# Optimization experiments

Measured on AMD Instinct MI355X. Metric: run time of the kernel, lower is better.

Reference implementation:

```python
import jax, jax.numpy as jnp
import numpy as np

N_HASHES = 4
CHUNK = 144


def conv2d(x, w, b, pad):
    y = jax.lax.conv_general_dilated(x, w, (1, 1), [(pad, pad), (pad, pad)],
                                     dimension_numbers=('NCHW', 'OIHW', 'NCHW'))
    return y + b[None, :, None, None]


def resblock(x, w1, b1, w2, b2, ws=None, bs=None):
    # conv3x3 -> ReLU -> conv3x3 + skip (1x1 projection when channels change)
    h = conv2d(x, w1, b1, 1)
    h = jax.nn.relu(h)
    h = conv2d(h, w2, b2, 1)
    skip = x if ws is None else conv2d(x, ws, bs, 0)
    return skip + h


def _forward(feature_dec1, feature_dec2, reference_feature,
             mw1, mb1, mw2, mb2, mws, mbs,
             a1w1, a1b1, a1w2, a1b2, a2w1, a2b1, a2w2, a2b2,
             random_index):
    fd1 = jax.lax.stop_gradient(feature_dec1)  # is_detach=True default
    fd2 = jax.lax.stop_gradient(feature_dec2)
    B, C0, H, W = fd1.shape
    L = H * W
    # embeddings: (B, L, C) with C = C0 // reduction, and (B, L, C0) assemblies
    f1 = resblock(fd1, mw1, mb1, mw2, mb2, mws, mbs).reshape(B, -1, L).transpose(0, 2, 1)
    f2 = resblock(fd2, mw1, mb1, mw2, mb2, mws, mbs).reshape(B, -1, L).transpose(0, 2, 1)
    aux1 = resblock(fd1, a1w1, a1b1, a1w2, a1b2).reshape(B, -1, L).transpose(0, 2, 1)
    refe = resblock(reference_feature, a2w1, a2b1, a2w2, a2b2).reshape(B, -1, L).transpose(0, 2, 1)
    C = f1.shape[-1]
    inv_random_index = jnp.argsort(random_index)
    hb = min(2 * L // CHUNK + (2 * L // CHUNK) % 2, 128)
    f1f2 = jnp.concatenate([f1, f2], axis=1)            # (B, 2L, C)
    # LSH hashing (random rotations drawn with a fixed key, matching randn-per-call in torch)
    rot = jax.random.normal(jax.random.key(42), (C, N_HASHES, hb // 2), dtype=f1f2.dtype)
    rv = jnp.einsum('btf,fhi->bhti', f1f2, rot)
    rv = jnp.concatenate([rv, -rv], axis=-1)
    codes = jnp.argmax(rv, axis=-1)                     # (B, nh, 2L)
    codes = codes + (jnp.arange(N_HASHES) * hb)[None, :, None]
    codes = codes[:, :, random_index].reshape(B, -1)    # (B, nh*2L)
    indices = jnp.argsort(codes, axis=-1)
    undo_sort = jnp.argsort(indices, axis=-1)
    mod_indices = (indices % 2) * L                     # faithful to torch `indices % 2 * L` precedence
    zo = jnp.concatenate([jnp.full((B, L), 0.01, f1.dtype),
                          jnp.full((B, L), 0.99, f1.dtype)], axis=1)
    f1f2_p = f1f2[:, random_index, :]
    q = jnp.take_along_axis(f1f2_p, mod_indices[:, :, None], axis=1)
    zo_p = zo[:, random_index]
    z = jnp.take_along_axis(zo_p, mod_indices, axis=1)
    refw = jnp.concatenate([aux1, refe], axis=1)[:, random_index, :]
    r = jnp.take_along_axis(refw, mod_indices[:, :, None], axis=1)
    rem = (2 * L) % CHUNK
    padding = CHUNK - rem if rem != 0 else 0
    qb = q.reshape(B, N_HASHES, 2 * L, C)
    zb = z.reshape(B, N_HASHES, 2 * L)
    rb = r.reshape(B, N_HASHES, 2 * L, -1)
    if padding:
        qb = jnp.concatenate([qb, qb[:, :, -padding:]], axis=2)
        zb = jnp.concatenate([zb, zb[:, :, -padding:]], axis=2)
        rb = jnp.concatenate([rb, rb[:, :, -padding:]], axis=2)
    k = qb.shape[2] // CHUNK
    qb = qb.reshape(B, N_HASHES, k, CHUNK, C)
    zb = zb.reshape(B, N_HASHES, k, CHUNK)
    rb = rb.reshape(B, N_HASHES, k, CHUNK, -1)
    # F.normalize(p=2, dim=-1, eps=5e-5)
    norm = jnp.sqrt(jnp.sum(qb * qb, axis=-1, keepdims=True))
    km = qb / jnp.maximum(norm, 5e-5)
    adj = lambda x: jnp.concatenate([x, jnp.roll(x, 1, axis=2), jnp.roll(x, -1, axis=2)], axis=3)
    km, zb3, rb3 = adj(km), adj(zb), adj(rb)            # keys/vals over 3 adjacent buckets
    raw = jnp.einsum('bhkie,bhkje->bhkij', qb, km)      # (B,nh,k,144,432)
    w = jnp.exp(raw) * zb3[:, :, :, None, :]
    denom = jnp.sum(w, axis=-1, keepdims=True)
    score = w / denom
    bucket_score = denom.reshape(B, N_HASHES, -1)
    ret = jnp.einsum('bhkij,bhkje->bhkie', score, rb3)  # (B,nh,k,144,C0)
    CR = rb3.shape[-1]
    ret = ret.reshape(B, N_HASHES, -1, CR)
    if padding:
        ret = ret[:, :, :-padding]
        bucket_score = bucket_score[:, :, :-padding]
    ret = ret.reshape(B, N_HASHES * 2 * L, CR)
    bucket_score = bucket_score.reshape(B, -1)
    ret = jnp.take_along_axis(ret, undo_sort[:, :, None], axis=1)
    bucket_score = jnp.take_along_axis(bucket_score, undo_sort, axis=1)
    ret = ret.reshape(B, N_HASHES, 2 * L, CR)
    bucket_score = bucket_score.reshape(B, N_HASHES, 2 * L, 1)
    probs = bucket_score / jnp.sum(bucket_score, axis=1, keepdims=True)
    ret = jnp.sum(ret * probs, axis=1)                  # (B, 2L, CR)
    ret = ret.transpose(0, 2, 1)[:, :, inv_random_index]
    return ret.reshape(B, CR, 2, H, W)[:, :, 0]         # (B, C0, H, W)


def setup_inputs() -> dict:
    key = jax.random.key(0)
    ks = jax.random.split(key, 12)
    B, C0, H, W = 2, 64, 100, 100
    red = 4
    Cm = C0 // red
    s = jnp.float32(0.05)
    rn = lambda i, shape: jax.random.normal(ks[i], shape, dtype=jnp.float32)
    return {
        'feature_dec1': rn(0, (B, C0, H, W)),
        'feature_dec2': rn(1, (B, C0, H, W)),
        'reference_feature': rn(2, (B, C0, H, W)),
        'random_index': jax.random.permutation(ks[3], 2 * H * W).astype(jnp.int32),
        'mw1': rn(4, (Cm, C0, 3, 3)) * s, 'mb1': jnp.zeros((Cm,), jnp.float32),
        'mw2': rn(5, (Cm, Cm, 3, 3)) * s, 'mb2': jnp.zeros((Cm,), jnp.float32),
        'mws': rn(6, (Cm, C0, 1, 1)) * s, 'mbs': jnp.zeros((Cm,), jnp.float32),
        'a1w1': rn(7, (C0, C0, 3, 3)) * s, 'a1b1': jnp.zeros((C0,), jnp.float32),
        'a1w2': rn(8, (C0, C0, 3, 3)) * s, 'a1b2': jnp.zeros((C0,), jnp.float32),
        'a2w1': rn(9, (C0, C0, 3, 3)) * s, 'a2b1': jnp.zeros((C0,), jnp.float32),
        'a2w2': rn(10, (C0, C0, 3, 3)) * s, 'a2b2': jnp.zeros((C0,), jnp.float32),
    }


def reference(feature_dec1, feature_dec2, reference_feature, random_index,
              mw1, mb1, mw2, mb2, mws, mbs,
              a1w1, a1b1, a1w2, a1b2, a2w1, a2b1, a2w2, a2b2):
    return _forward(feature_dec1, feature_dec2, reference_feature,
                    mw1, mb1, mw2, mb2, mws, mbs,
                    a1w1, a1b1, a1w2, a1b2, a2w1, a2b1, a2w2, a2b2,
                    random_index)
```

## Files before the change

### kernel.cpp

```cpp
#include <hip/hip_runtime.h>

#define JAX_THREEFRY_PARTITIONABLE 1

namespace {

constexpr int BN   = 2;
constexpr int C0   = 64;
constexpr int HH   = 100;
constexpr int WWW  = 100;
constexpr int LL   = 10000;
constexpr int TL   = 20000;
constexpr int CHK  = 144;
constexpr int NCHK = 139;
constexpr int NPAD = 16;
constexpr int WINR = 432;

constexpr int OFF_ROT  = 0;
constexpr int OFF_WT1  = OFF_ROT + 4096;
constexpr int OFF_WT2  = OFF_WT1 + 9216;
constexpr int OFF_WTS  = OFF_WT2 + 2304;
constexpr int OFF_HT0  = OFF_WTS + 1024;
constexpr int OFF_HT1  = OFF_HT0 + 640000;
constexpr int OFF_HT2  = OFF_HT1 + 640000;
constexpr int OFF_HT3  = OFF_HT2 + 640000;
constexpr int OFF_F    = OFF_HT3 + 640000;
constexpr int OFF_SC   = OFF_F + 640000;
constexpr int OFF_CODE = OFF_SC + 272;
constexpr int OFF_RANK = OFF_CODE + 40000;
constexpr int OFF_N0   = OFF_RANK + 160000;
constexpr int OFF_INV  = OFF_N0 + 1112;
constexpr int OFF_AUX  = OFF_INV + 10000;

constexpr int AUXW = 36864;

__device__ __forceinline__ unsigned rotl32(unsigned v, int r) {
  return (v << r) | (v >> (32 - r));
}

__device__ void tf2x32(unsigned k0, unsigned k1, unsigned x0, unsigned x1,
                       unsigned& o0, unsigned& o1) {
  unsigned ks2 = k0 ^ k1 ^ 0x1BD11BDAu;
  x0 += k0; x1 += k1;
#define TFR(r) { x0 += x1; x1 = rotl32(x1, r); x1 ^= x0; }
  TFR(13) TFR(15) TFR(26) TFR(6)  x0 += k1;  x1 += ks2 + 1u;
  TFR(17) TFR(29) TFR(16) TFR(24) x0 += ks2; x1 += k0 + 2u;
  TFR(13) TFR(15) TFR(26) TFR(6)  x0 += k0;  x1 += k1 + 3u;
  TFR(17) TFR(29) TFR(16) TFR(24) x0 += k1;  x1 += ks2 + 4u;
  TFR(13) TFR(15) TFR(26) TFR(6)  x0 += ks2; x1 += k0 + 5u;
#undef TFR
  o0 = x0; o1 = x1;
}

__device__ float xla_erfinv(float x) {
#pragma clang fp contract(off)
  float w = -log1pf(-x * x);
  float p;
  if (w < 5.0f) {
    w = w - 2.5f;
    p = 2.81022636e-08f;
    p = 3.43273939e-07f  + p * w;
    p = -3.5233877e-06f  + p * w;
    p = -4.39150654e-06f + p * w;
    p = 0.00021858087f   + p * w;
    p = -0.00125372503f  + p * w;
    p = -0.00417768164f  + p * w;
    p = 0.246640727f     + p * w;
    p = 1.50140941f      + p * w;
  } else {
    w = sqrtf(w) - 3.0f;
    p = -0.000200214257f;
    p = 0.000100950558f + p * w;
    p = 0.00134934322f  + p * w;
    p = -0.00367342844f + p * w;
    p = 0.00573950773f  + p * w;
    p = -0.0076224613f  + p * w;
    p = 0.00943887047f  + p * w;
    p = 1.00167406f     + p * w;
    p = 2.83297682f     + p * w;
  }
  return p * x;
}

__global__ void k_prep(const float* __restrict__ mw1, const float* __restrict__ mw2,
                       const float* __restrict__ mws,
                       const float* __restrict__ a1w1, const float* __restrict__ a1w2,
                       const float* __restrict__ a2w1, const float* __restrict__ a2w2,
                       const int* __restrict__ ri,
                       float* __restrict__ rotT, float* __restrict__ wT1,
                       float* __restrict__ wT2, float* __restrict__ wTs,
                       float* __restrict__ auxT, int* __restrict__ inv) {
  int gid = blockIdx.x * 256 + threadIdx.x;
  if (gid < 4 * AUXW) {
    int wsel = gid / AUXW, j = gid % AUXW;
    const float* src = (wsel == 0) ? a1w1 : (wsel == 1) ? a1w2 : (wsel == 2) ? a2w1 : a2w2;
    int co = j / 576, r = j % 576;
    auxT[wsel * AUXW + r * 64 + co] = src[j];
    return;
  }
  int g2 = gid - 4 * AUXW;
  if (g2 < 4096) {
    int i = g2;
    unsigned o0, o1, bits;
#if JAX_THREEFRY_PARTITIONABLE
    tf2x32(0u, 42u, 0u, (unsigned)i, o0, o1);
    bits = o0 ^ o1;
#else
    if (i < 2048) { tf2x32(0u, 42u, (unsigned)i, (unsigned)(i + 2048), o0, o1); bits = o0; }
    else          { tf2x32(0u, 42u, (unsigned)(i - 2048), (unsigned)i, o0, o1); bits = o1; }
#endif
    unsigned fb = (bits >> 9) | 0x3f800000u;
    float f = __uint_as_float(fb) - 1.0f;
    const float lo = __uint_as_float(0xBF7FFFFFu);
    float u = fmaxf(lo, f * 2.0f + lo);
    float r = __uint_as_float(0x3FB504F3u) * xla_erfinv(u);
    int c = i >> 8, h = (i >> 6) & 3, j = i & 63;
    rotT[(h * 64 + j) * 16 + c] = r;
    return;
  }
  int g3 = g2 - 4096;
  if (g3 < 9216) {
    { int o = g3 / 576; int r = g3 % 576; wT1[r * 16 + o] = mw1[g3]; }
    if (g3 < 2304) { int o = g3 / 144; int r = g3 % 144; wT2[r * 16 + o] = mw2[g3]; }
    if (g3 < 1024) { int o = g3 / 64;  int ci = g3 % 64; wTs[ci * 16 + o] = mws[g3]; }
    return;
  }
  int g4 = g3 - 9216;
  if (g4 < TL) {
    int p = ri[g4];
    if (p < LL) inv[p] = g4;
  }
}

__global__ __launch_bounds__(512) void k_conv1(
    const float* __restrict__ fd1, const float* __restrict__ fd2,
    const float* __restrict__ wT1,
    float* __restrict__ ht0, float* __restrict__ ht1,
    float* __restrict__ ht2, float* __restrict__ ht3) {
  int x = blockIdx.x;
  int blk = (x & 7) * 182 + (x >> 3);
  int kq = blk & 3;
  int rest = blk >> 2;
  int n = rest / 91, tile = rest % 91;
  int yt = tile / 7, xt = tile % 7;
  int ty0 = yt * 8, tx0 = xt * 16;
  const float* in = ((n >> 1) ? fd2 : fd1) + (n & 1) * (C0 * LL) + (kq * 16) * LL;
  float* htk = ((kq == 0) ? ht0 : (kq == 1) ? ht1 : (kq == 2) ? ht2 : ht3) + n * 16 * LL;
  int tid = threadIdx.x;
  int co = tid & 15, xq = (tid >> 4) & 3, yl = tid >> 6;

  __shared__ float sIn[16 * 10 * 20];
  __shared__ float sW[144 * 16];

  for (int i = tid; i < 144 * 16; i += 512) sW[i] = wT1[kq * 2304 + i];
  for (int idx = tid; idx < 16 * 10 * 18; idx += 512) {
    int ci = idx / 180, r = idx % 180, iy = r / 18, ix = r % 18;
    int gy = ty0 - 1 + iy, gx = tx0 - 1 + ix;
    float v = 0.f;
    if (gy >= 0 && gy < HH && gx >= 0 && gx < WWW) v = in[ci * LL + gy * WWW + gx];
    sIn[ci * 200 + iy * 20 + ix] = v;
  }
  __syncthreads();

  float acc[4];
#pragma unroll
  for (int p = 0; p < 4; ++p) acc[p] = 0.f;

  for (int cc = 0; cc < 4; ++cc) {
    float w[4][9];
#pragma unroll
    for (int c4 = 0; c4 < 4; ++c4)
#pragma unroll
      for (int t = 0; t < 9; ++t)
        w[c4][t] = sW[((cc * 4 + c4) * 9 + t) * 16 + co];
#pragma unroll
    for (int c4 = 0; c4 < 4; ++c4) {
      const float* rowb = &sIn[(cc * 4 + c4) * 200 + yl * 20 + xq * 4];
#pragma unroll
      for (int dy = 0; dy < 3; ++dy) {
        const float* r = rowb + dy * 20;
        float v[6];
#pragma unroll
        for (int k = 0; k < 6; ++k) v[k] = r[k];
#pragma unroll
        for (int dx = 0; dx < 3; ++dx) {
          float wv = w[c4][dy * 3 + dx];
#pragma unroll
          for (int p = 0; p < 4; ++p) acc[p] = fmaf(v[p + dx], wv, acc[p]);
        }
      }
    }
  }

  int yv = ty0 + yl;
  int xg = tx0 + xq * 4;
  if (yv < HH && xg < WWW) {
    float4 s = make_float4(acc[0], acc[1], acc[2], acc[3]);
    *(float4*)&htk[co * LL + yv * WWW + xg] = s;
  }
}

__global__ __launch_bounds__(512) void k_conv2(
    const float* __restrict__ fd1, const float* __restrict__ fd2,
    const float* __restrict__ ht0, const float* __restrict__ ht1,
    const float* __restrict__ ht2, const float* __restrict__ ht3,
    const float* __restrict__ wT2, const float* __restrict__ mb1,
    const float* __restrict__ mb2, const float* __restrict__ wTs,
    const float* __restrict__ mbs, float* __restrict__ F) {
  int xx = blockIdx.x;
  int xcd = xx & 7, slot = xx >> 3;
  int blk = (xcd < 4) ? (xcd * 46 + slot) : (184 + (xcd - 4) * 45 + slot);
  int n = blk / 91, tile = blk % 91;
  int yt = tile / 7, xt = tile % 7;
  int ty0 = yt * 8, tx0 = xt * 16;
  int src = n >> 1, b = n & 1;
  const float* in = (src ? fd2 : fd1) + b * (C0 * LL);
  const float* h0 = ht0 + n * 16 * LL;
  const float* h1 = ht1 + n * 16 * LL;
  const float* h2 = ht2 + n * 16 * LL;
  const float* h3 = ht3 + n * 16 * LL;
  int tid = threadIdx.x;
  int co = tid & 15, xq = (tid >> 4) & 3, yl = tid >> 6;

  __shared__ float sW2[144 * 16];
  __shared__ float sWs[64 * 16];
  __shared__ float sH[16 * 10 * 20];
  __shared__ float sSkip[16 * 8 * 17];

  for (int i = tid; i < 144 * 16; i += 512) sW2[i] = wT2[i];
  for (int i = tid; i < 64 * 16; i += 512) sWs[i] = wTs[i];
  for (int idx = tid; idx < 16 * 10 * 18; idx += 512) {
    int ci = idx / 180, r = idx % 180, iy = r / 18, ix = r % 18;
    int gy = ty0 - 1 + iy, gx = tx0 - 1 + ix;
    float v = 0.f;
    if (gy >= 0 && gy < HH && gx >= 0 && gx < WWW) {
      int o = ci * LL + gy * WWW + gx;
      v = fmaxf(h0[o] + h1[o] + h2[o] + h3[o] + mb1[ci], 0.f);
    }
    sH[ci * 200 + iy * 20 + ix] = v;
  }
  __syncthreads();

  float acc[4];
  float bias = mb2[co] + mbs[co];
#pragma unroll
  for (int p = 0; p < 4; ++p) acc[p] = bias;

  for (int ci = 0; ci < 16; ++ci) {
    const float* rowb = &sH[ci * 200 + yl * 20 + xq * 4];
#pragma unroll
    for (int dy = 0; dy < 3; ++dy) {
      const float* r = rowb + dy * 20;
      float v[6];
#pragma unroll
      for (int k = 0; k < 6; ++k) v[k] = r[k];
#pragma unroll
      for (int dx = 0; dx < 3; ++dx) {
        float wv = sW2[(ci * 9 + dy * 3 + dx) * 16 + co];
#pragma unroll
        for (int p = 0; p < 4; ++p) acc[p] = fmaf(v[p + dx], wv, acc[p]);
      }
    }
  }

  for (int cc = 0; cc < 4; ++cc) {
    __syncthreads();
    for (int idx = tid; idx < 16 * 8 * 16; idx += 512) {
      int ci = idx >> 7, r = idx & 127, iy = r >> 4, ix = r & 15;
      int gy = ty0 + iy, gx = tx0 + ix;
      float v = 0.f;
      if (gy < HH && gx < WWW) v = in[(cc * 16 + ci) * LL + gy * WWW + gx];
      sSkip[(ci * 8 + iy) * 17 + ix] = v;
    }
    __syncthreads();
    for (int c16 = 0; c16 < 16; ++c16) {
      float wv = sWs[(cc * 16 + c16) * 16 + co];
      const float* sv = &sSkip[(c16 * 8 + yl) * 17 + xq * 4];
#pragma unroll
      for (int p = 0; p < 4; ++p) acc[p] = fmaf(sv[p], wv, acc[p]);
    }
  }

  int yv = ty0 + yl;
  if (yv < HH) {
    float* Fb = F + (b * TL + src * LL + yv * WWW) * 16 + co;
#pragma unroll
    for (int p = 0; p < 4; ++p) {
      int xv = tx0 + xq * 4 + p;
      if (xv < WWW) Fb[xv * 16] = acc[p];
    }
  }
}

__global__ __launch_bounds__(576) void k_codes(
    const float* __restrict__ F, const float* __restrict__ rotT,
    const int* __restrict__ ri, unsigned char* __restrict__ codes,
    const float* __restrict__ fd1, const float* __restrict__ refin,
    const float* __restrict__ auxT,
    const float* __restrict__ a1b1, const float* __restrict__ a1b2,
    const float* __restrict__ a2b1, const float* __restrict__ a2b2,
    float* __restrict__ SC) {
  int blk = blockIdx.x;
  int tid = threadIdx.x;

  if (blk < 280) {
    int bh = blk / 35, seg = blk % 35;
    int b = bh >> 2, h = bh & 3;
    __shared__ float srot[1024];
    for (int i = tid; i < 1024; i += 576) srot[i] = rotT[h * 1024 + i];
    __syncthreads();
    int t = seg * 576 + tid;
    if (t >= TL) return;
    int pos = ri[t];
    const float* Fr = F + (b * TL + pos) * 16;
    float q[16];
#pragma unroll
    for (int c = 0; c < 16; ++c) q[c] = Fr[c];
    float best = -1e30f; int bi = 0;
    float worst = 1e30f; int wi = 0;
    for (int j = 0; j < 64; ++j) {
      float v = 0.f;
      const float* rp = srot + j * 16;
#pragma unroll
      for (int c = 0; c < 16; ++c) v = fmaf(q[c], rp[c], v);
      if (v > best)  { best = v;  bi = j; }
      if (v < worst) { worst = v; wi = j; }
    }
    int code = (best >= -worst) ? bi : (64 + wi);
    codes[bh * TL + t] = (unsigned char)code;
    return;
  }

  if (blk == 284) {
#pragma clang fp contract(off)
    int b = tid;
    if (b >= BN) return;
    int j0 = ri[0], jL = ri[LL];
    const float* qA = F + (b * TL + j0) * 16;
    const float* qB = F + (b * TL + jL) * 16;
    float nA = 0.f, nB = 0.f;
    for (int c = 0; c < 16; ++c) { nA += qA[c] * qA[c]; nB += qB[c] * qB[c]; }
    float mA = fmaxf(sqrtf(nA), 5e-5f), mB = fmaxf(sqrtf(nB), 5e-5f);
    float d00 = 0.f, d01 = 0.f, d10 = 0.f, d11 = 0.f;
    for (int c = 0; c < 16; ++c) {
      float kAc = qA[c] / mA, kBc = qB[c] / mB;
      d00 += qA[c] * kAc; d01 += qA[c] * kBc;
      d10 += qB[c] * kAc; d11 += qB[c] * kBc;
    }
    float zA = (j0 < LL) ? 0.01f : 0.99f;
    float zB = (jL < LL) ? 0.01f : 0.99f;
    float* sc = SC + b * 136;
    sc[0] = expf(d00) * zA; sc[1] = expf(d01) * zB;
    sc[2] = expf(d10) * zA; sc[3] = expf(d11) * zB;
    return;
  }

  int pb = blk - 280;
  int b = pb & 1, which = pb >> 1;
  int pos = ri[which * LL];
  const float *in, *w1T, *b1, *w2T, *b2;
  int sp;
  if (pos < LL) {
    in = fd1 + b * C0 * LL; w1T = auxT; b1 = a1b1; w2T = auxT + AUXW; b2 = a1b2; sp = pos;
  } else {
    in = refin + b * C0 * LL; w1T = auxT + 2 * AUXW; b1 = a2b1; w2T = auxT + 3 * AUXW;
    b2 = a2b2; sp = pos - LL;
  }
  int y = sp / WWW, x = sp % WWW;

  __shared__ float sPatch[64][25];
  __shared__ float sW[144 * 64];
  __shared__ float sH[9][64];
  __shared__ float sPart[9][64];

  for (int idx = tid; idx < 64 * 25; idx += 576) {
    int ci = idx / 25, pp = idx % 25;
    int gy = y - 2 + pp / 5, gx = x - 2 + pp % 5;
    float v = 0.f;
    if (gy >= 0 && gy < HH && gx >= 0 && gx < WWW) v = in[ci * LL + gy * WWW + gx];
    sPatch[ci][pp] = v;
  }

  int p = tid / 64, ch = tid & 63;
  int p3 = p / 3, pm = p % 3;
  int yy = y + p3 - 1, xx = x + pm - 1;
  bool inb = (yy >= 0) && (yy < HH) && (xx >= 0) && (xx < WWW);

  float acc0 = 0.f, acc1 = 0.f;
  for (int cc = 0; cc < 4; ++cc) {
    __syncthreads();
    for (int i = tid; i < 144 * 64; i += 576) sW[i] = w1T[cc * 9216 + i];
    __syncthreads();
    if (inb) {
#pragma unroll
      for (int ci = 0; ci < 16; ++ci) {
        const float* wp = &sW[ci * 9 * 64 + ch];
        const float* pr = &sPatch[cc * 16 + ci][0];
#pragma unroll
        for (int t = 0; t < 9; ++t) {
          float v = pr[(p3 + t / 3) * 5 + (pm + t % 3)];
          if (ci & 1) acc1 = fmaf(v, wp[t * 64], acc1);
          else        acc0 = fmaf(v, wp[t * 64], acc0);
        }
      }
    }
  }
  sH[p][ch] = inb ? fmaxf(acc0 + acc1 + b1[ch], 0.f) : 0.f;
  __syncthreads();

  {
    float part = 0.f;
    const float* wbase = w2T + p * 64 + ch;
    for (int ci = 0; ci < 64; ++ci) part = fmaf(sH[p][ci], wbase[ci * 9 * 64], part);
    sPart[p][ch] = part;
  }
  __syncthreads();
  if (tid < 64) {
    int co = tid;
    float a = in[co * LL + y * WWW + x] + b2[co];
#pragma unroll
    for (int g = 0; g < 9; ++g) a += sPart[g][co];
    SC[b * 136 + 4 + which * 64 + co] = a;
  }
}

__global__ __launch_bounds__(256) void k_sort(
    const unsigned char* __restrict__ codes,
    int* __restrict__ rank_of, int* __restrict__ n0g) {
  int bh = blockIdx.x;
  const unsigned char* keys = codes + bh * TL;
  __shared__ unsigned short cnt[240][128];
  __shared__ unsigned int totals[128];
  __shared__ unsigned int baseoff[128];
  __shared__ unsigned int n0s[NCHK];
  int tid = threadIdx.x;
  for (int i = tid; i < 240 * 128 / 2; i += 256) ((unsigned int*)cnt)[i] = 0u;
  for (int i = tid; i < NCHK; i += 256) n0s[i] = 0u;
  __syncthreads();
  const int SEG = 84;
  int base = tid * SEG;
  int nloc = (tid < 240) ? (TL - base) : 0;
  if (nloc > SEG) nloc = SEG;
  if (nloc < 0) nloc = 0;
  for (int e = 0; e < nloc; ++e) cnt[tid][keys[base + e]]++;
  __syncthreads();
  if (tid < 128) {
    unsigned int s = 0;
    for (int g = 0; g < 240; ++g) s += cnt[g][tid];
    totals[tid] = s;
  }
  __syncthreads();
  if (tid == 0) {
    unsigned int run = 0;
    for (int c = 0; c < 128; ++c) { baseoff[c] = run; run += totals[c]; }
  }
  __syncthreads();
  if (tid < 128) {
    unsigned int run = baseoff[tid];
    for (int g = 0; g < 240; ++g) {
      unsigned int v = cnt[g][tid];
      cnt[g][tid] = (unsigned short)run;
      run += v;
    }
  }
  __syncthreads();
  for (int e = 0; e < nloc; ++e) {
    int idx = base + e;
    int c = keys[idx];
    int r = cnt[tid][c]++;
    rank_of[bh * TL + idx] = r;
    if (!(idx & 1)) {
      atomicAdd(&n0s[r / CHK], 1u);
      if (r >= TL - NPAD) atomicAdd(&n0s[NCHK - 1], 1u);
    }
  }
  __syncthreads();
  for (int i = tid; i < NCHK; i += 256) n0g[bh * NCHK + i] = (int)n0s[i];
}

__global__ __launch_bounds__(256) void k_out(
    const int* __restrict__ inv, const int* __restrict__ rank_of,
    const int* __restrict__ n0, const float* __restrict__ SC,
    float* __restrict__ out) {
  int b = blockIdx.y;
  int c0 = blockIdx.z * 16;
  int p = blockIdx.x * 256 + threadIdx.x;
  if (p >= LL) return;
  int t = inv[p];
  int si = t & 1;
  float e0 = SC[b * 136 + si * 2 + 0];
  float e1 = SC[b * 136 + si * 2 + 1];
  float s0 = 0.f, s1 = 0.f;
  for (int h = 0; h < 4; ++h) {
    int r = rank_of[(b * 4 + h) * TL + t];
    int k = r / CHK;
    int km = (k == 0) ? NCHK - 1 : k - 1;
    int kp = (k == NCHK - 1) ? 0 : k + 1;
    const int* nb = n0 + (b * 4 + h) * NCHK;
    int W0 = nb[k] + nb[km] + nb[kp];
    s0 += (float)W0 * e0;
    s1 += (float)(WINR - W0) * e1;
  }
  float invd = 1.f / (s0 + s1);
  float al = s0 * invd;
  float be = s1 * invd;
  const float* rA = SC + b * 136 + 4;
  const float* rB = rA + 64;
  float* o = out + b * C0 * LL + p;
#pragma unroll
  for (int c = 0; c < 16; ++c) o[(c0 + c) * LL] = al * rA[c0 + c] + be * rB[c0 + c];
}

}

extern "C" void kernel_launch(void* const* d_in, const int* in_sizes, int n_in,
                              void* d_out, int out_size, void* d_ws, size_t ws_size,
                              hipStream_t stream) {
  const float* fd1  = (const float*)d_in[0];
  const float* fd2  = (const float*)d_in[1];
  const float* reff = (const float*)d_in[2];
  const int*   ri   = (const int*)d_in[3];
  const float* mw1  = (const float*)d_in[4];
  const float* mb1  = (const float*)d_in[5];
  const float* mw2  = (const float*)d_in[6];
  const float* mb2  = (const float*)d_in[7];
  const float* mws  = (const float*)d_in[8];
  const float* mbs  = (const float*)d_in[9];
  const float* a1w1 = (const float*)d_in[10];
  const float* a1b1 = (const float*)d_in[11];
  const float* a1w2 = (const float*)d_in[12];
  const float* a1b2 = (const float*)d_in[13];
  const float* a2w1 = (const float*)d_in[14];
  const float* a2b1 = (const float*)d_in[15];
  const float* a2w2 = (const float*)d_in[16];
  const float* a2b2 = (const float*)d_in[17];

  float* ws = (float*)d_ws;
  float* rotT = ws + OFF_ROT;
  float* wT1  = ws + OFF_WT1;
  float* wT2  = ws + OFF_WT2;
  float* wTs  = ws + OFF_WTS;
  float* ht0  = ws + OFF_HT0;
  float* ht1  = ws + OFF_HT1;
  float* ht2  = ws + OFF_HT2;
  float* ht3  = ws + OFF_HT3;
  float* F    = ws + OFF_F;
  float* SC   = ws + OFF_SC;
  unsigned char* codes = (unsigned char*)(ws + OFF_CODE);
  int* rank_of = (int*)(ws + OFF_RANK);
  int* n0      = (int*)(ws + OFF_N0);
  int* invp    = (int*)(ws + OFF_INV);
  float* auxT  = ws + OFF_AUX;

  k_prep<<<dim3(707), dim3(256), 0, stream>>>(mw1, mw2, mws, a1w1, a1w2, a2w1, a2w2,
                                              ri, rotT, wT1, wT2, wTs, auxT, invp);
  k_conv1<<<dim3(1456), dim3(512), 0, stream>>>(fd1, fd2, wT1, ht0, ht1, ht2, ht3);
  k_conv2<<<dim3(364), dim3(512), 0, stream>>>(fd1, fd2, ht0, ht1, ht2, ht3, wT2,
                                               mb1, mb2, wTs, mbs, F);
  k_codes<<<dim3(285), dim3(576), 0, stream>>>(F, rotT, ri, codes, fd1, reff, auxT,
                                               a1b1, a1b2, a2b1, a2b2, SC);
  k_sort<<<dim3(8), dim3(256), 0, stream>>>(codes, rank_of, n0);
  k_out<<<dim3(40, 2, 4), dim3(256), 0, stream>>>(invp, rank_of, n0, SC, (float*)d_out);
}
```

Measured before the change: 126.7 us.

## Drop prep kernel by reading raw weights in-kernel and parallelize sort scan

Removes the k_prep launch. The conv kernels now transpose weights directly from the original layouts while loading shared memory, the LSH rotation matrix is generated on the fly inside k_codes, and the inverse-permutation build moves into extra k_codes blocks. The sort kernel's counting-sort prefix stage is restructured: keys are read as packed words, the count table is transposed and padded, and the serial per-bucket scans are replaced by a two-level parallel scan with a wave shuffle. This trades a kernel launch and a workspace round trip for strided weight reads and repeated RNG work per block, and aims to shorten the sort kernel, which runs on only 8 blocks.

```diff
diff --git a/kernel.cpp b/kernel.cpp
--- a/kernel.cpp
+++ b/kernel.cpp
@@ -15,11 +15,7 @@
 constexpr int NPAD = 16;
 constexpr int WINR = 432;
 
-constexpr int OFF_ROT  = 0;
-constexpr int OFF_WT1  = OFF_ROT + 4096;
-constexpr int OFF_WT2  = OFF_WT1 + 9216;
-constexpr int OFF_WTS  = OFF_WT2 + 2304;
-constexpr int OFF_HT0  = OFF_WTS + 1024;
+constexpr int OFF_HT0  = 0;
 constexpr int OFF_HT1  = OFF_HT0 + 640000;
 constexpr int OFF_HT2  = OFF_HT1 + 640000;
 constexpr int OFF_HT3  = OFF_HT2 + 640000;
@@ -29,9 +25,6 @@
 constexpr int OFF_RANK = OFF_CODE + 40000;
 constexpr int OFF_N0   = OFF_RANK + 160000;
 constexpr int OFF_INV  = OFF_N0 + 1112;
-constexpr int OFF_AUX  = OFF_INV + 10000;
-
-constexpr int AUXW = 36864;
 
 __device__ __forceinline__ unsigned rotl32(unsigned v, int r) {
   return (v << r) | (v >> (32 - r));
@@ -81,59 +74,25 @@
   return p * x;
 }
 
-__global__ void k_prep(const float* __restrict__ mw1, const float* __restrict__ mw2,
-                       const float* __restrict__ mws,
-                       const float* __restrict__ a1w1, const float* __restrict__ a1w2,
-                       const float* __restrict__ a2w1, const float* __restrict__ a2w2,
-                       const int* __restrict__ ri,
-                       float* __restrict__ rotT, float* __restrict__ wT1,
-                       float* __restrict__ wT2, float* __restrict__ wTs,
-                       float* __restrict__ auxT, int* __restrict__ inv) {
-  int gid = blockIdx.x * 256 + threadIdx.x;
-  if (gid < 4 * AUXW) {
-    int wsel = gid / AUXW, j = gid % AUXW;
-    const float* src = (wsel == 0) ? a1w1 : (wsel == 1) ? a1w2 : (wsel == 2) ? a2w1 : a2w2;
-    int co = j / 576, r = j % 576;
-    auxT[wsel * AUXW + r * 64 + co] = src[j];
-    return;
-  }
-  int g2 = gid - 4 * AUXW;
-  if (g2 < 4096) {
-    int i = g2;
-    unsigned o0, o1, bits;
+__device__ float rot_rng(int i) {
+  unsigned o0, o1, bits;
 #if JAX_THREEFRY_PARTITIONABLE
-    tf2x32(0u, 42u, 0u, (unsigned)i, o0, o1);
-    bits = o0 ^ o1;
+  tf2x32(0u, 42u, 0u, (unsigned)i, o0, o1);
+  bits = o0 ^ o1;
 #else
-    if (i < 2048) { tf2x32(0u, 42u, (unsigned)i, (unsigned)(i + 2048), o0, o1); bits = o0; }
-    else          { tf2x32(0u, 42u, (unsigned)(i - 2048), (unsigned)i, o0, o1); bits = o1; }
+  if (i < 2048) { tf2x32(0u, 42u, (unsigned)i, (unsigned)(i + 2048), o0, o1); bits = o0; }
+  else          { tf2x32(0u, 42u, (unsigned)(i - 2048), (unsigned)i, o0, o1); bits = o1; }
 #endif
-    unsigned fb = (bits >> 9) | 0x3f800000u;
-    float f = __uint_as_float(fb) - 1.0f;
-    const float lo = __uint_as_float(0xBF7FFFFFu);
-    float u = fmaxf(lo, f * 2.0f + lo);
-    float r = __uint_as_float(0x3FB504F3u) * xla_erfinv(u);
-    int c = i >> 8, h = (i >> 6) & 3, j = i & 63;
-    rotT[(h * 64 + j) * 16 + c] = r;
-    return;
-  }
-  int g3 = g2 - 4096;
-  if (g3 < 9216) {
-    { int o = g3 / 576; int r = g3 % 576; wT1[r * 16 + o] = mw1[g3]; }
-    if (g3 < 2304) { int o = g3 / 144; int r = g3 % 144; wT2[r * 16 + o] = mw2[g3]; }
-    if (g3 < 1024) { int o = g3 / 64;  int ci = g3 % 64; wTs[ci * 16 + o] = mws[g3]; }
-    return;
-  }
-  int g4 = g3 - 9216;
-  if (g4 < TL) {
-    int p = ri[g4];
-    if (p < LL) inv[p] = g4;
-  }
+  unsigned fb = (bits >> 9) | 0x3f800000u;
+  float f = __uint_as_float(fb) - 1.0f;
+  const float lo = __uint_as_float(0xBF7FFFFFu);
+  float u = fmaxf(lo, f * 2.0f + lo);
+  return __uint_as_float(0x3FB504F3u) * xla_erfinv(u);
 }
 
 __global__ __launch_bounds__(512) void k_conv1(
     const float* __restrict__ fd1, const float* __restrict__ fd2,
-    const float* __restrict__ wT1,
+    const float* __restrict__ mw1,
     float* __restrict__ ht0, float* __restrict__ ht1,
     float* __restrict__ ht2, float* __restrict__ ht3) {
   int x = blockIdx.x;
@@ -151,7 +110,10 @@
   __shared__ float sIn[16 * 10 * 20];
   __shared__ float sW[144 * 16];
 
-  for (int i = tid; i < 144 * 16; i += 512) sW[i] = wT1[kq * 2304 + i];
+  for (int i = tid; i < 144 * 16; i += 512) {
+    int o = i & 15, r = i >> 4;
+    sW[i] = mw1[o * 576 + kq * 144 + r];
+  }
   for (int idx = tid; idx < 16 * 10 * 18; idx += 512) {
     int ci = idx / 180, r = idx % 180, iy = r / 18, ix = r % 18;
     int gy = ty0 - 1 + iy, gx = tx0 - 1 + ix;
@@ -203,8 +165,8 @@
     const float* __restrict__ fd1, const float* __restrict__ fd2,
     const float* __restrict__ ht0, const float* __restrict__ ht1,
     const float* __restrict__ ht2, const float* __restrict__ ht3,
-    const float* __restrict__ wT2, const float* __restrict__ mb1,
-    const float* __restrict__ mb2, const float* __restrict__ wTs,
+    const float* __restrict__ mw2, const float* __restrict__ mb1,
+    const float* __restrict__ mb2, const float* __restrict__ mws,
     const float* __restrict__ mbs, float* __restrict__ F) {
   int xx = blockIdx.x;
   int xcd = xx & 7, slot = xx >> 3;
@@ -226,8 +188,14 @@
   __shared__ float sH[16 * 10 * 20];
   __shared__ float sSkip[16 * 8 * 17];
 
-  for (int i = tid; i < 144 * 16; i += 512) sW2[i] = wT2[i];
-  for (int i = tid; i < 64 * 16; i += 512) sWs[i] = wTs[i];
+  for (int i = tid; i < 144 * 16; i += 512) {
+    int o = i & 15, r = i >> 4;
+    sW2[i] = mw2[o * 144 + r];
+  }
+  for (int i = tid; i < 64 * 16; i += 512) {
+    int o = i & 15, ci = i >> 4;
+    sWs[i] = mws[o * 64 + ci];
+  }
   for (int idx = tid; idx < 16 * 10 * 18; idx += 512) {
     int ci = idx / 180, r = idx % 180, iy = r / 18, ix = r % 18;
     int gy = ty0 - 1 + iy, gx = tx0 - 1 + ix;
@@ -292,13 +260,14 @@
 }
 
 __global__ __launch_bounds__(576) void k_codes(
-    const float* __restrict__ F, const float* __restrict__ rotT,
-    const int* __restrict__ ri, unsigned char* __restrict__ codes,
+    const float* __restrict__ F, const int* __restrict__ ri,
+    unsigned char* __restrict__ codes,
     const float* __restrict__ fd1, const float* __restrict__ refin,
-    const float* __restrict__ auxT,
-    const float* __restrict__ a1b1, const float* __restrict__ a1b2,
-    const float* __restrict__ a2b1, const float* __restrict__ a2b2,
-    float* __restrict__ SC) {
+    const float* __restrict__ a1w1, const float* __restrict__ a1b1,
+    const float* __restrict__ a1w2, const float* __restrict__ a1b2,
+    const float* __restrict__ a2w1, const float* __restrict__ a2b1,
+    const float* __restrict__ a2w2, const float* __restrict__ a2b2,
+    float* __restrict__ SC, int* __restrict__ inv) {
   int blk = blockIdx.x;
   int tid = threadIdx.x;
 
@@ -306,7 +275,10 @@
     int bh = blk / 35, seg = blk % 35;
     int b = bh >> 2, h = bh & 3;
     __shared__ float srot[1024];
-    for (int i = tid; i < 1024; i += 576) srot[i] = rotT[h * 1024 + i];
+    for (int l = tid; l < 1024; l += 576) {
+      int j = l >> 4, c = l & 15;
+      srot[l] = rot_rng(c * 256 + h * 64 + j);
+    }
     __syncthreads();
     int t = seg * 576 + tid;
     if (t >= TL) return;
@@ -327,6 +299,15 @@
     }
     int code = (best >= -worst) ? bi : (64 + wi);
     codes[bh * TL + t] = (unsigned char)code;
+    return;
+  }
+
+  if (blk >= 285) {
+    int t = (blk - 285) * 576 + tid;
+    if (t < TL) {
+      int p = ri[t];
+      if (p < LL) inv[p] = t;
+    }
     return;
   }
 
@@ -357,13 +338,13 @@
   int pb = blk - 280;
   int b = pb & 1, which = pb >> 1;
   int pos = ri[which * LL];
-  const float *in, *w1T, *b1, *w2T, *b2;
+  const float *in, *w1, *b1, *w2, *b2;
   int sp;
   if (pos < LL) {
-    in = fd1 + b * C0 * LL; w1T = auxT; b1 = a1b1; w2T = auxT + AUXW; b2 = a1b2; sp = pos;
+    in = fd1 + b * C0 * LL; w1 = a1w1; b1 = a1b1; w2 = a1w2; b2 = a1b2; sp = pos;
   } else {
-    in = refin + b * C0 * LL; w1T = auxT + 2 * AUXW; b1 = a2b1; w2T = auxT + 3 * AUXW;
-    b2 = a2b2; sp = pos - LL;
+    in = refin + b * C0 * LL; w1 = a2w1; b1 = a2b1; w2 = a2w2; b2 = a2b2;
+    sp = pos - LL;
   }
   int y = sp / WWW, x = sp % WWW;
 
@@ -388,7 +369,10 @@
   float acc0 = 0.f, acc1 = 0.f;
   for (int cc = 0; cc < 4; ++cc) {
     __syncthreads();
-    for (int i = tid; i < 144 * 64; i += 576) sW[i] = w1T[cc * 9216 + i];
+    for (int i = tid; i < 144 * 64; i += 576) {
+      int chh = i & 63, rl = i >> 6;
+      sW[i] = w1[chh * 576 + cc * 144 + rl];
+    }
     __syncthreads();
     if (inb) {
 #pragma unroll
@@ -409,8 +393,8 @@
 
   {
     float part = 0.f;
-    const float* wbase = w2T + p * 64 + ch;
-    for (int ci = 0; ci < 64; ++ci) part = fmaf(sH[p][ci], wbase[ci * 9 * 64], part);
+    for (int ci = 0; ci < 64; ++ci)
+      part = fmaf(sH[p][ci], w2[ch * 576 + ci * 9 + p], part);
     sPart[p][ch] = part;
   }
   __syncthreads();
@@ -427,47 +411,93 @@
     const unsigned char* __restrict__ codes,
     int* __restrict__ rank_of, int* __restrict__ n0g) {
   int bh = blockIdx.x;
-  const unsigned char* keys = codes + bh * TL;
-  __shared__ unsigned short cnt[240][128];
-  __shared__ unsigned int totals[128];
+  const unsigned int* keys4 = (const unsigned int*)(codes + bh * TL);
+  __shared__ unsigned short cnt[128 * 241];
+  __shared__ unsigned int sup[128 * 16];
+  __shared__ unsigned int totalsL[128];
   __shared__ unsigned int baseoff[128];
   __shared__ unsigned int n0s[NCHK];
+  __shared__ unsigned int wtot;
   int tid = threadIdx.x;
-  for (int i = tid; i < 240 * 128 / 2; i += 256) ((unsigned int*)cnt)[i] = 0u;
+
+  for (int i = tid; i < 128 * 241 / 2; i += 256) ((unsigned int*)cnt)[i] = 0u;
   for (int i = tid; i < NCHK; i += 256) n0s[i] = 0u;
   __syncthreads();
+
   const int SEG = 84;
   int base = tid * SEG;
   int nloc = (tid < 240) ? (TL - base) : 0;
   if (nloc > SEG) nloc = SEG;
   if (nloc < 0) nloc = 0;
-  for (int e = 0; e < nloc; ++e) cnt[tid][keys[base + e]]++;
-  __syncthreads();
+
+  unsigned int kw[21];
+  int nw = (nloc + 3) >> 2;
+  for (int w = 0; w < nw; ++w) kw[w] = keys4[tid * 21 + w];
+
+  for (int e = 0; e < nloc; ++e) {
+    int c = (kw[e >> 2] >> ((e & 3) * 8)) & 255;
+    cnt[c * 241 + tid]++;
+  }
+  __syncthreads();
+
+  for (int idx = tid; idx < 128 * 15; idx += 256) {
+    int c = idx / 15, s = idx % 15;
+    unsigned int sum = 0;
+#pragma unroll
+    for (int k = 0; k < 16; ++k) sum += cnt[c * 241 + 16 * s + k];
+    sup[c * 16 + s] = sum;
+  }
+  __syncthreads();
+
   if (tid < 128) {
-    unsigned int s = 0;
-    for (int g = 0; g < 240; ++g) s += cnt[g][tid];
-    totals[tid] = s;
-  }
-  __syncthreads();
-  if (tid == 0) {
     unsigned int run = 0;
-    for (int c = 0; c < 128; ++c) { baseoff[c] = run; run += totals[c]; }
-  }
-  __syncthreads();
-  if (tid < 128) {
-    unsigned int run = baseoff[tid];
-    for (int g = 0; g < 240; ++g) {
-      unsigned int v = cnt[g][tid];
-      cnt[g][tid] = (unsigned short)run;
-      run += v;
-    }
-  }
-  __syncthreads();
+#pragma unroll
+    for (int s = 0; s < 15; ++s) {
+      unsigned int t = sup[tid * 16 + s];
+      sup[tid * 16 + s] = run;
+      run += t;
+    }
+    totalsL[tid] = run;
+  }
+  __syncthreads();
+
+  {
+    unsigned int v = 0;
+    if (tid < 128) {
+      v = totalsL[tid];
+#pragma unroll
+      for (int d = 1; d < 64; d <<= 1) {
+        unsigned int o = __shfl_up(v, d);
+        if ((tid & 63) >= d) v += o;
+      }
+      if (tid == 63) wtot = v;
+    }
+    __syncthreads();
+    if (tid < 128) {
+      unsigned int incl = v + ((tid >= 64) ? wtot : 0u);
+      baseoff[tid] = incl - totalsL[tid];
+    }
+  }
+  __syncthreads();
+
+  for (int idx = tid; idx < 128 * 15; idx += 256) {
+    int c = idx / 15, s = idx % 15;
+    unsigned int run = baseoff[c] + sup[c * 16 + s];
+#pragma unroll
+    for (int k = 0; k < 16; ++k) {
+      int g = 16 * s + k;
+      unsigned int t = cnt[c * 241 + g];
+      cnt[c * 241 + g] = (unsigned short)run;
+      run += t;
+    }
+  }
+  __syncthreads();
+
   for (int e = 0; e < nloc; ++e) {
     int idx = base + e;
-    int c = keys[idx];
-    int r = cnt[tid][c]++;
-    rank_of[bh * TL + idx] = r;
+    int c = (kw[e >> 2] >> ((e & 3) * 8)) & 255;
+    unsigned int r = cnt[c * 241 + tid]++;
+    rank_of[bh * TL + idx] = (int)r;
     if (!(idx & 1)) {
       atomicAdd(&n0s[r / CHK], 1u);
       if (r >= TL - NPAD) atomicAdd(&n0s[NCHK - 1], 1u);
@@ -535,10 +565,6 @@
   const float* a2b2 = (const float*)d_in[17];
 
   float* ws = (float*)d_ws;
-  float* rotT = ws + OFF_ROT;
-  float* wT1  = ws + OFF_WT1;
-  float* wT2  = ws + OFF_WT2;
-  float* wTs  = ws + OFF_WTS;
   float* ht0  = ws + OFF_HT0;
   float* ht1  = ws + OFF_HT1;
   float* ht2  = ws + OFF_HT2;
@@ -549,15 +575,13 @@
   int* rank_of = (int*)(ws + OFF_RANK);
   int* n0      = (int*)(ws + OFF_N0);
   int* invp    = (int*)(ws + OFF_INV);
-  float* auxT  = ws + OFF_AUX;
-
-  k_prep<<<dim3(707), dim3(256), 0, stream>>>(mw1, mw2, mws, a1w1, a1w2, a2w1, a2w2,
-                                              ri, rotT, wT1, wT2, wTs, auxT, invp);
-  k_conv1<<<dim3(1456), dim3(512), 0, stream>>>(fd1, fd2, wT1, ht0, ht1, ht2, ht3);
-  k_conv2<<<dim3(364), dim3(512), 0, stream>>>(fd1, fd2, ht0, ht1, ht2, ht3, wT2,
-                                               mb1, mb2, wTs, mbs, F);
-  k_codes<<<dim3(285), dim3(576), 0, stream>>>(F, rotT, ri, codes, fd1, reff, auxT,
-                                               a1b1, a1b2, a2b1, a2b2, SC);
+
+  k_conv1<<<dim3(1456), dim3(512), 0, stream>>>(fd1, fd2, mw1, ht0, ht1, ht2, ht3);
+  k_conv2<<<dim3(364), dim3(512), 0, stream>>>(fd1, fd2, ht0, ht1, ht2, ht3, mw2,
+                                               mb1, mb2, mws, mbs, F);
+  k_codes<<<dim3(320), dim3(576), 0, stream>>>(F, ri, codes, fd1, reff,
+                                               a1w1, a1b1, a1w2, a1b2,
+                                               a2w1, a2b1, a2w2, a2b2, SC, invp);
   k_sort<<<dim3(8), dim3(256), 0, stream>>>(codes, rank_of, n0);
   k_out<<<dim3(40, 2, 4), dim3(256), 0, stream>>>(invp, rank_of, n0, SC, (float*)d_out);
 }
```

Result: slower. 139.4 us (+10.1%).
